# Optimization experiments

Measured on AMD Instinct MI355X. Metric: run time of the kernel, lower is better.

## Reference

```python
import jax, jax.numpy as jnp
import numpy as np

NPG = 128      # nodes per graph = g(4) * e(32), forced by rearrange + cnn1 channels
G, E32 = 4, 32
ALPHA = 1.0    # GCN2Conv(in_channels, 1) -> alpha = 1
BETA = 1.0     # theta=None -> beta = 1


def _gcn_norm(edge_index, edge_weight, n):
    """PyG gcn_norm: add self-loops (w=1), sym-normalize by degree at dst."""
    src, dst = edge_index[0], edge_index[1]
    loop = jnp.arange(n)
    src = jnp.concatenate([src, loop])
    dst = jnp.concatenate([dst, loop])
    w = jnp.concatenate([edge_weight, jnp.ones((n,), edge_weight.dtype)])
    deg = jax.ops.segment_sum(w, dst, num_segments=n)
    dinv = jnp.where(deg > 0, jax.lax.rsqrt(deg), 0.0)
    norm = dinv[src] * w * dinv[dst]
    return src, dst, norm


def _propagate(x, src, dst, norm, n):
    # gather -> weight -> scatter-add (SpMM)
    return jax.ops.segment_sum(x[src] * norm[:, None], dst, num_segments=n)


def setup_inputs() -> dict:
    key = jax.random.key(0)
    ks = jax.random.split(key, 10)
    N, E, C, H, CH = 65536, 524288, 128, 512, 256
    x = jax.random.normal(ks[0], (N, C), jnp.float32)
    edge_index = jax.random.randint(ks[1], (2, E), 0, N, dtype=jnp.int64)
    edge_attr = jax.random.uniform(ks[2], (E,), jnp.float32)
    w1_gcn2 = jax.random.normal(ks[3], (C, C), jnp.float32) / np.float32(np.sqrt(C))
    w_gcn = jax.random.normal(ks[4], (C, H), jnp.float32) / np.float32(np.sqrt(C))
    b_gcn = jnp.zeros((H,), jnp.float32)
    w_cnn1 = jax.random.normal(ks[5], (H, 4 * H), jnp.float32) / np.float32(np.sqrt(4 * H))
    b_cnn1 = jnp.zeros((H,), jnp.float32)
    w_cnn2 = jax.random.normal(ks[6], (CH, H), jnp.float32) / np.float32(np.sqrt(H))
    b_cnn2 = jnp.zeros((CH,), jnp.float32)
    w_lin = jax.random.normal(ks[7], (32 * CH,), jnp.float32) / np.float32(np.sqrt(32 * CH))
    b_lin = jnp.zeros((), jnp.float32)
    return {"x": x, "edge_attr": edge_attr, "w1_gcn2": w1_gcn2, "w_gcn": w_gcn,
            "b_gcn": b_gcn, "w_cnn1": w_cnn1, "b_cnn1": b_cnn1, "w_cnn2": w_cnn2,
            "b_cnn2": b_cnn2, "w_lin": w_lin, "b_lin": b_lin, "edge_index": edge_index}


def reference(x, edge_attr, w1_gcn2, w_gcn, b_gcn, w_cnn1, b_cnn1, w_cnn2, b_cnn2,
              w_lin, b_lin, edge_index):
    n = x.shape[0]
    bs = n // NPG
    src, dst, norm = _gcn_norm(edge_index, edge_attr, n)

    # GCN2Conv(C, layer=1): h = (1-a)*A_hat x + a*x0; out = (1-b)*h + b*(h @ W1)
    h = _propagate(x, src, dst, norm, n)
    h = h * (1.0 - ALPHA) + ALPHA * x
    h = (1.0 - BETA) * h + BETA * (h @ w1_gcn2)

    # GCNConv(C, H): A_hat (h @ W) + b
    h = _propagate(h @ w_gcn, src, dst, norm, n) + b_gcn
    h = jnp.tanh(h)

    f = h.shape[1]  # hidden_channels
    # '(bs g e) f -> bs (g f) e', e=32, g=4
    h = h.reshape(bs, G, E32, f).transpose(0, 1, 3, 2).reshape(bs, G * f, E32)
    # 1x1 convs == per-position linears over channel dim
    h = jax.nn.relu(jnp.einsum('bce,oc->boe', h, w_cnn1) + b_cnn1[None, :, None])
    h = jax.nn.relu(jnp.einsum('bce,oc->boe', h, w_cnn2) + b_cnn2[None, :, None])
    # dropout p=0.5 is identity in eval mode
    h = h.reshape(bs, -1)
    out = h @ w_lin + b_lin
    return jax.nn.sigmoid(out)
```

## Files before the change

kernel.cpp:

```cpp
#include <hip/hip_runtime.h>
#include <hip/hip_bf16.h>

#define N_NODES 65536
#define N_EDGES 524288

typedef __attribute__((ext_vector_type(8))) short bf16x8;
typedef __attribute__((ext_vector_type(4))) float f32x4;

__device__ __forceinline__ float bf2f(unsigned short u) {
    union { unsigned int i; float f; } v;
    v.i = ((unsigned int)u) << 16;
    return v.f;
}
__device__ __forceinline__ unsigned short f2bf(float f) {
    union { float f; unsigned int i; } v;
    v.f = f;
    unsigned int r = v.i + 0x7fff + ((v.i >> 16) & 1);
    return (unsigned short)(r >> 16);
}

__global__ void init_k(int* __restrict__ cnt, float* __restrict__ logits) {
    int i = blockIdx.x * 256 + threadIdx.x;
    cnt[i] = 0;
    if (i < 512) logits[i] = 0.0f;
}
__global__ void cnt_k(const int* __restrict__ dst, int* __restrict__ cnt) {
    int e = blockIdx.x * 256 + threadIdx.x;
    atomicAdd(&cnt[dst[e]], 1);
}

__global__ __launch_bounds__(256) void scan1_k(const int* __restrict__ cnt,
                                               int* __restrict__ rp,
                                               int* __restrict__ bsum) {
    __shared__ int s[256];
    int t = threadIdx.x, g = blockIdx.x * 256 + t;
    int v = cnt[g];
    s[t] = v;
    __syncthreads();
    for (int d = 1; d < 256; d <<= 1) {
        int u = (t >= d) ? s[t - d] : 0;
        __syncthreads();
        s[t] += u;
        __syncthreads();
    }
    rp[g] = s[t] - v;
    if (t == 255) bsum[blockIdx.x] = s[255];
}
__global__ __launch_bounds__(256) void scan2_k(int* __restrict__ bsum,
                                               int* __restrict__ rp) {
    __shared__ int s[256];
    int t = threadIdx.x;
    int v = bsum[t];
    s[t] = v;
    __syncthreads();
    for (int d = 1; d < 256; d <<= 1) {
        int u = (t >= d) ? s[t - d] : 0;
        __syncthreads();
        s[t] += u;
        __syncthreads();
    }
    bsum[t] = s[t] - v;
    if (t == 255) rp[65536] = s[255];
}
__global__ __launch_bounds__(256) void scan3_k(int* __restrict__ rp,
                                               const int* __restrict__ bsum,
                                               int* __restrict__ cursor) {
    int t = threadIdx.x, g = blockIdx.x * 256 + t;
    int r = rp[g] + bsum[blockIdx.x];
    rp[g] = r;
    cursor[g] = r;
}

__global__ void scatter_k(const int* __restrict__ src, const int* __restrict__ dst,
                          const float* __restrict__ w,
                          int* __restrict__ cursor, uint2* __restrict__ ep) {
    int e = blockIdx.x * 256 + threadIdx.x;
    int pos = atomicAdd(&cursor[dst[e]], 1);
    uint2 p;
    p.x = (unsigned int)src[e];
    p.y = __float_as_uint(w[e]);
    ep[pos] = p;
}

__global__ void rowsum_k(const int* __restrict__ rp, const uint2* __restrict__ ep,
                         float* __restrict__ dinv) {
    int n = blockIdx.x * 256 + threadIdx.x;
    int beg = rp[n], end = rp[n + 1];
    float s = 1.0f;
    for (int i = beg; i < end; ++i) s += __uint_as_float(ep[i].y);
    dinv[n] = rsqrtf(s);
}

__global__ void xscale_k(const float* __restrict__ x, const float* __restrict__ dinv,
                         __hip_bfloat16* __restrict__ xbf) {
    int i = (blockIdx.x * 256 + threadIdx.x) * 4;
    float d = dinv[i >> 7];
    float4 v = *(const float4*)(x + i);
    alignas(8) __hip_bfloat16 tmp[4] = {
        __float2bfloat16(d * v.x), __float2bfloat16(d * v.y),
        __float2bfloat16(d * v.z), __float2bfloat16(d * v.w)};
    *(ushort4*)((unsigned short*)xbf + i) = *(const ushort4*)tmp;
}

__global__ void wprep_k(const float* __restrict__ wc1, __hip_bfloat16* __restrict__ wc1bf,
                        const float* __restrict__ wc2, __hip_bfloat16* __restrict__ wc2bf,
                        const float* __restrict__ w1, const float* __restrict__ wg,
                        __hip_bfloat16* __restrict__ WT) {
    int bid = blockIdx.x;
    if (bid < 1152) {
        const float* in;
        __hip_bfloat16* outp;
        int i;
        if (bid < 1024) { in = wc1; outp = wc1bf; i = bid * 1024 + threadIdx.x * 4; }
        else            { in = wc2; outp = wc2bf; i = (bid - 1024) * 1024 + threadIdx.x * 4; }
        float4 v = *(const float4*)(in + i);
        alignas(8) __hip_bfloat16 tmp[4] = {__float2bfloat16(v.x), __float2bfloat16(v.y),
                                            __float2bfloat16(v.z), __float2bfloat16(v.w)};
        *(ushort4*)((unsigned short*)outp + i) = *(const ushort4*)tmp;
    } else {
        int t = (bid - 1152) * 256 + threadIdx.x;
        int f = t >> 7, c = t & 127;
        float s = 0.f;
#pragma unroll 8
        for (int m = 0; m < 128; ++m) s += w1[c * 128 + m] * wg[m * 512 + f];
        WT[t] = __float2bfloat16(s);
    }
}

__global__ __launch_bounds__(256) void gather_k(const int* __restrict__ rp,
                                                const uint2* __restrict__ ep,
                                                const unsigned short* __restrict__ xbf,
                                                const float* __restrict__ dinv,
                                                __hip_bfloat16* __restrict__ ybf) {
    int n = (blockIdx.x * 256 + threadIdx.x) >> 6;
    int lane = threadIdx.x & 63;
    int beg = rp[n], end = rp[n + 1];
    float accx, accy;
    {
        unsigned int u = *(const unsigned int*)(xbf + (size_t)n * 128 + lane * 2);
        accx = bf2f((unsigned short)(u & 0xffff));
        accy = bf2f((unsigned short)(u >> 16));
    }
    int i = beg;
    for (; i + 8 <= end; i += 8) {
        uint2 p[8];
        unsigned int u[8];
#pragma unroll
        for (int k = 0; k < 8; ++k) p[k] = ep[i + k];
#pragma unroll
        for (int k = 0; k < 8; ++k)
            u[k] = *(const unsigned int*)(xbf + (size_t)p[k].x * 128 + lane * 2);
#pragma unroll
        for (int k = 0; k < 8; ++k) {
            float c = __uint_as_float(p[k].y);
            accx += c * bf2f((unsigned short)(u[k] & 0xffff));
            accy += c * bf2f((unsigned short)(u[k] >> 16));
        }
    }
    for (; i + 4 <= end; i += 4) {
        uint2 p[4];
        unsigned int u[4];
#pragma unroll
        for (int k = 0; k < 4; ++k) p[k] = ep[i + k];
#pragma unroll
        for (int k = 0; k < 4; ++k)
            u[k] = *(const unsigned int*)(xbf + (size_t)p[k].x * 128 + lane * 2);
#pragma unroll
        for (int k = 0; k < 4; ++k) {
            float c = __uint_as_float(p[k].y);
            accx += c * bf2f((unsigned short)(u[k] & 0xffff));
            accy += c * bf2f((unsigned short)(u[k] >> 16));
        }
    }
    for (; i < end; ++i) {
        uint2 p = ep[i];
        unsigned int u = *(const unsigned int*)(xbf + (size_t)p.x * 128 + lane * 2);
        float c = __uint_as_float(p.y);
        accx += c * bf2f((unsigned short)(u & 0xffff));
        accy += c * bf2f((unsigned short)(u >> 16));
    }
    float dn = dinv[n];
    accx *= dn;
    accy *= dn;
    alignas(4) __hip_bfloat16 o[2] = {__float2bfloat16(accx), __float2bfloat16(accy)};
    *(unsigned int*)((unsigned short*)ybf + (size_t)n * 128 + lane * 2) =
        *(const unsigned int*)o;
}

__device__ __forceinline__ void gll16(const void* g, void* l) {
    __builtin_amdgcn_global_load_lds(
        (const __attribute__((address_space(1))) void*)g,
        (__attribute__((address_space(3))) void*)l, 16, 0, 0);
}

template <int ACT, int OUT_MODE, int SWIZ_NTX>
__global__ __launch_bounds__(256) void gemm_mfma_k(
    const __hip_bfloat16* __restrict__ A, const __hip_bfloat16* __restrict__ B,
    const float* __restrict__ bias, void* __restrict__ Cout,
    const float* __restrict__ wlin, int M, int N, int K) {
    __shared__ char lds[65536];

    const int tid = threadIdx.x;
    const int lane = tid & 63, wid = tid >> 6;
    int bx, by;
    if (SWIZ_NTX > 0) {
        int orig = blockIdx.x;
        int per = gridDim.x / (8 * SWIZ_NTX);
        int xcd = orig & 7, k = orig >> 3;
        by = xcd * per + k / SWIZ_NTX;
        bx = k % SWIZ_NTX;
    } else {
        bx = blockIdx.x;
        by = blockIdx.y;
    }
    const int bm = by * 128, bn = bx * 128;
    const int wr = wid >> 1, wc = wid & 1;

    const int srow = wid * 16 + (lane >> 2);
    const int skcol = (((lane & 3) ^ ((lane >> 3) & 3))) * 8;
    const __hip_bfloat16* Abase = A + (size_t)(bm + srow) * K + skcol;
    const __hip_bfloat16* Bbase = B + (size_t)(bn + srow) * K + skcol;
    const int ldso = wid * 1024;

    f32x4 acc[4][4] = {};

    const int lrow = lane & 15;
    const int lkb = (((lane >> 4) ^ ((lane >> 1) & 3)) << 4);
    const int nk = K >> 5;

    auto stage = [&](int buf, int kt) {
        char* la = lds + buf * 16384;
        char* lb = la + 8192;
        gll16(Abase + kt * 32,                  la + ldso);
        gll16(Abase + kt * 32 + (size_t)64 * K, la + 4096 + ldso);
        gll16(Bbase + kt * 32,                  lb + ldso);
        gll16(Bbase + kt * 32 + (size_t)64 * K, lb + 4096 + ldso);
    };

    stage(0, 0);
    stage(1, 1);
    stage(2, 2);

    for (int kt = 0; kt < nk; ++kt) {
        int ahead = nk - 1 - kt;
        if (ahead >= 2)      asm volatile("s_waitcnt vmcnt(8)" ::: "memory");
        else if (ahead == 1) asm volatile("s_waitcnt vmcnt(4)" ::: "memory");
        else                 asm volatile("s_waitcnt vmcnt(0)" ::: "memory");
        __builtin_amdgcn_s_barrier();
        asm volatile("" ::: "memory");
        if (kt + 3 < nk) stage((kt + 3) & 3, kt + 3);

        const char* la = lds + (kt & 3) * 16384;
        const char* lb = la + 8192;
        bf16x8 af[4], bfr[4];
#pragma unroll
        for (int i = 0; i < 4; ++i)
            af[i] = *(const bf16x8*)(la + (wr * 64 + i * 16 + lrow) * 64 + lkb);
#pragma unroll
        for (int j = 0; j < 4; ++j)
            bfr[j] = *(const bf16x8*)(lb + (wc * 64 + j * 16 + lrow) * 64 + lkb);
        __builtin_amdgcn_s_setprio(1);
#pragma unroll
        for (int i = 0; i < 4; ++i)
#pragma unroll
            for (int j = 0; j < 4; ++j)
                acc[i][j] = __builtin_amdgcn_mfma_f32_16x16x32_bf16(
                    bfr[j], af[i], acc[i][j], 0, 0, 0);
        __builtin_amdgcn_s_setprio(0);
        asm volatile("" ::: "memory");
    }

    const int l15 = lane & 15, lhi = lane >> 4;

    if (OUT_MODE == 3) {
        float p0 = 0.f, p1 = 0.f;
#pragma unroll
        for (int i = 0; i < 4; ++i) {
            int e = (i & 1) * 16 + l15;
#pragma unroll
            for (int j = 0; j < 4; ++j) {
                int n = bn + wc * 64 + j * 16 + lhi * 4;
                float4 bv = *(const float4*)(bias + n);
#pragma unroll
                for (int r = 0; r < 4; ++r) {
                    float v = fmaxf(acc[i][j][r] + ((const float*)&bv)[r], 0.f);
                    float wl = wlin[(n + r) * 32 + e];
                    if (i < 2) p0 += v * wl; else p1 += v * wl;
                }
            }
        }
#pragma unroll
        for (int off = 32; off > 0; off >>= 1) {
            p0 += __shfl_down(p0, off, 64);
            p1 += __shfl_down(p1, off, 64);
        }
        if (lane == 0) {
            int g = (bm >> 5) + wr * 2;
            atomicAdd(&((float*)Cout)[g], p0);
            atomicAdd(&((float*)Cout)[g + 1], p1);
        }
        return;
    }

#pragma unroll
    for (int i = 0; i < 4; ++i) {
        int m = bm + wr * 64 + i * 16 + l15;
#pragma unroll
        for (int j = 0; j < 4; ++j) {
            int n = bn + wc * 64 + j * 16 + lhi * 4;
            float4 bv = *(const float4*)(bias + n);
            ushort4 o;
#pragma unroll
            for (int r = 0; r < 4; ++r) {
                float v = acc[i][j][r] + ((const float*)&bv)[r];
                if (ACT == 1) v = fmaxf(v, 0.f);
                if (ACT == 2) v = 1.0f - 2.0f / (__expf(2.0f * v) + 1.0f);
                ((unsigned short*)&o)[r] = f2bf(v);
            }
            if (OUT_MODE == 1) {
                *(ushort4*)((unsigned short*)Cout + (size_t)m * N + n) = o;
            } else {
                size_t prow = (size_t)(((m >> 7) << 5) | (m & 31));
                size_t idx = prow * 2048 + (size_t)(((m >> 5) & 3) * 512 + n);
                *(ushort4*)((unsigned short*)Cout + idx) = o;
            }
        }
    }
}

__global__ void sigmoid_k(const float* __restrict__ logits,
                          const float* __restrict__ blin, float* __restrict__ out) {
    int b = blockIdx.x * 256 + threadIdx.x;
    out[b] = 1.0f / (1.0f + expf(-(logits[b] + blin[0])));
}

extern "C" void kernel_launch(void* const* d_in, const int* in_sizes, int n_in,
                              void* d_out, int out_size, void* d_ws, size_t ws_size,
                              hipStream_t stream) {
    const float* x    = (const float*)d_in[0];
    const float* eattr= (const float*)d_in[1];
    const float* w1   = (const float*)d_in[2];
    const float* wg   = (const float*)d_in[3];
    const float* bg   = (const float*)d_in[4];
    const float* wc1  = (const float*)d_in[5];
    const float* bc1  = (const float*)d_in[6];
    const float* wc2  = (const float*)d_in[7];
    const float* bc2  = (const float*)d_in[8];
    const float* wlin = (const float*)d_in[9];
    const float* blin = (const float*)d_in[10];
    const int*   ei   = (const int*)d_in[11];
    const int* esrc = ei;
    const int* edst = ei + N_EDGES;
    float* out = (float*)d_out;

    char* ws = (char*)d_ws;
    float*          dinv   = (float*)(ws + 0);
    int*            cnt    = (int*)(ws + 262144);
    int*            rp     = (int*)(ws + 524288);
    int*            cursor = (int*)(ws + 786688);
    uint2*          ep     = (uint2*)(ws + 1048832);
    __hip_bfloat16* WTbf   = (__hip_bfloat16*)(ws + 5243136);
    __hip_bfloat16* ybf    = (__hip_bfloat16*)(ws + 5374208);
    __hip_bfloat16* V      = (__hip_bfloat16*)(ws + 22151424);
    __hip_bfloat16* act1   = (__hip_bfloat16*)(ws + 89260288);
    __hip_bfloat16* wc1bf  = (__hip_bfloat16*)(ws + 106037504);
    __hip_bfloat16* wc2bf  = (__hip_bfloat16*)(ws + 108134656);
    __hip_bfloat16* xbf    = (__hip_bfloat16*)(ws + 108396800);
    float*          logits = (float*)(ws + 125174016);
    int*            bsum   = (int*)(ws + 125176064);
    if (ws_size < (size_t)125177088) return;

    init_k<<<N_NODES / 256, 256, 0, stream>>>(cnt, logits);

    cnt_k<<<N_EDGES / 256, 256, 0, stream>>>(edst, cnt);

    scan1_k<<<256, 256, 0, stream>>>(cnt, rp, bsum);
    scan2_k<<<1, 256, 0, stream>>>(bsum, rp);
    scan3_k<<<256, 256, 0, stream>>>(rp, bsum, cursor);

    scatter_k<<<N_EDGES / 256, 256, 0, stream>>>(esrc, edst, eattr, cursor, ep);

    rowsum_k<<<N_NODES / 256, 256, 0, stream>>>(rp, ep, dinv);

    wprep_k<<<1408, 256, 0, stream>>>(wc1, wc1bf, wc2, wc2bf, w1, wg, WTbf);
    xscale_k<<<(N_NODES * 128 / 4) / 256, 256, 0, stream>>>(x, dinv, xbf);

    gather_k<<<N_NODES / 4, 256, 0, stream>>>(rp, ep,
                                              (const unsigned short*)xbf, dinv, ybf);

    gemm_mfma_k<2, 2, 0><<<dim3(4, 512), 256, 0, stream>>>(
        ybf, WTbf, bg, V, nullptr, 65536, 512, 128);

    gemm_mfma_k<1, 1, 4><<<512, 256, 0, stream>>>(
        V, wc1bf, bc1, act1, nullptr, 16384, 512, 2048);

    gemm_mfma_k<1, 3, 0><<<dim3(2, 128), 256, 0, stream>>>(
        act1, wc2bf, bc2, logits, wlin, 16384, 256, 512);

    sigmoid_k<<<2, 256, 0, stream>>>(logits, blin, out);
}
```

Measured before the change: 212.7 us.

## Fuse SpMM gather with first GEMM, merge prep and rowsum/xscale kernels

```diff
diff --git a/kernel.cpp b/kernel.cpp
--- a/kernel.cpp
+++ b/kernel.cpp
@@ -24,9 +24,35 @@
     cnt[i] = 0;
     if (i < 512) logits[i] = 0.0f;
 }
-__global__ void cnt_k(const int* __restrict__ dst, int* __restrict__ cnt) {
-    int e = blockIdx.x * 256 + threadIdx.x;
-    atomicAdd(&cnt[dst[e]], 1);
+
+__global__ void prep1_k(const int* __restrict__ dst, int* __restrict__ cnt,
+                        const float* __restrict__ wc1, __hip_bfloat16* __restrict__ wc1bf,
+                        const float* __restrict__ wc2, __hip_bfloat16* __restrict__ wc2bf,
+                        const float* __restrict__ w1, const float* __restrict__ wg,
+                        __hip_bfloat16* __restrict__ WTpk) {
+    int bid = blockIdx.x;
+    if (bid < 2048) {
+        int e = bid * 256 + threadIdx.x;
+        atomicAdd(&cnt[dst[e]], 1);
+    } else if (bid < 3200) {
+        const float* in;
+        __hip_bfloat16* outp;
+        int i;
+        if (bid < 3072) { in = wc1; outp = wc1bf; i = (bid - 2048) * 1024 + threadIdx.x * 4; }
+        else            { in = wc2; outp = wc2bf; i = (bid - 3072) * 1024 + threadIdx.x * 4; }
+        float4 v = *(const float4*)(in + i);
+        alignas(8) __hip_bfloat16 tmp[4] = {__float2bfloat16(v.x), __float2bfloat16(v.y),
+                                            __float2bfloat16(v.z), __float2bfloat16(v.w)};
+        *(ushort4*)((unsigned short*)outp + i) = *(const ushort4*)tmp;
+    } else {
+        int t = (bid - 3200) * 256 + threadIdx.x;
+        int f = t >> 7, c = t & 127;
+        float s = 0.f;
+#pragma unroll 8
+        for (int m = 0; m < 128; ++m) s += w1[c * 128 + m] * wg[m * 512 + f];
+        int pk = ((((f >> 4) * 4 + (c >> 5)) * 64 + ((c >> 3) & 3) * 16 + (f & 15)) * 8) + (c & 7);
+        WTpk[pk] = __float2bfloat16(s);
+    }
 }
 
 __global__ __launch_bounds__(256) void scan1_k(const int* __restrict__ cnt,
@@ -82,109 +108,126 @@
     ep[pos] = p;
 }
 
-__global__ void rowsum_k(const int* __restrict__ rp, const uint2* __restrict__ ep,
-                         float* __restrict__ dinv) {
-    int n = blockIdx.x * 256 + threadIdx.x;
-    int beg = rp[n], end = rp[n + 1];
-    float s = 1.0f;
-    for (int i = beg; i < end; ++i) s += __uint_as_float(ep[i].y);
-    dinv[n] = rsqrtf(s);
-}
-
-__global__ void xscale_k(const float* __restrict__ x, const float* __restrict__ dinv,
-                         __hip_bfloat16* __restrict__ xbf) {
-    int i = (blockIdx.x * 256 + threadIdx.x) * 4;
-    float d = dinv[i >> 7];
-    float4 v = *(const float4*)(x + i);
-    alignas(8) __hip_bfloat16 tmp[4] = {
-        __float2bfloat16(d * v.x), __float2bfloat16(d * v.y),
-        __float2bfloat16(d * v.z), __float2bfloat16(d * v.w)};
-    *(ushort4*)((unsigned short*)xbf + i) = *(const ushort4*)tmp;
-}
-
-__global__ void wprep_k(const float* __restrict__ wc1, __hip_bfloat16* __restrict__ wc1bf,
-                        const float* __restrict__ wc2, __hip_bfloat16* __restrict__ wc2bf,
-                        const float* __restrict__ w1, const float* __restrict__ wg,
-                        __hip_bfloat16* __restrict__ WT) {
-    int bid = blockIdx.x;
-    if (bid < 1152) {
-        const float* in;
-        __hip_bfloat16* outp;
-        int i;
-        if (bid < 1024) { in = wc1; outp = wc1bf; i = bid * 1024 + threadIdx.x * 4; }
-        else            { in = wc2; outp = wc2bf; i = (bid - 1024) * 1024 + threadIdx.x * 4; }
-        float4 v = *(const float4*)(in + i);
-        alignas(8) __hip_bfloat16 tmp[4] = {__float2bfloat16(v.x), __float2bfloat16(v.y),
-                                            __float2bfloat16(v.z), __float2bfloat16(v.w)};
-        *(ushort4*)((unsigned short*)outp + i) = *(const ushort4*)tmp;
-    } else {
-        int t = (bid - 1152) * 256 + threadIdx.x;
-        int f = t >> 7, c = t & 127;
-        float s = 0.f;
-#pragma unroll 8
-        for (int m = 0; m < 128; ++m) s += w1[c * 128 + m] * wg[m * 512 + f];
-        WT[t] = __float2bfloat16(s);
-    }
-}
-
-__global__ __launch_bounds__(256) void gather_k(const int* __restrict__ rp,
-                                                const uint2* __restrict__ ep,
-                                                const unsigned short* __restrict__ xbf,
-                                                const float* __restrict__ dinv,
-                                                __hip_bfloat16* __restrict__ ybf) {
+__global__ __launch_bounds__(256) void rx_k(const int* __restrict__ rp,
+                                            const uint2* __restrict__ ep,
+                                            const float* __restrict__ x,
+                                            float* __restrict__ dinv,
+                                            __hip_bfloat16* __restrict__ xbf) {
     int n = (blockIdx.x * 256 + threadIdx.x) >> 6;
     int lane = threadIdx.x & 63;
     int beg = rp[n], end = rp[n + 1];
-    float accx, accy;
-    {
-        unsigned int u = *(const unsigned int*)(xbf + (size_t)n * 128 + lane * 2);
-        accx = bf2f((unsigned short)(u & 0xffff));
-        accy = bf2f((unsigned short)(u >> 16));
-    }
-    int i = beg;
-    for (; i + 8 <= end; i += 8) {
-        uint2 p[8];
-        unsigned int u[8];
-#pragma unroll
-        for (int k = 0; k < 8; ++k) p[k] = ep[i + k];
-#pragma unroll
-        for (int k = 0; k < 8; ++k)
-            u[k] = *(const unsigned int*)(xbf + (size_t)p[k].x * 128 + lane * 2);
-#pragma unroll
-        for (int k = 0; k < 8; ++k) {
-            float c = __uint_as_float(p[k].y);
-            accx += c * bf2f((unsigned short)(u[k] & 0xffff));
-            accy += c * bf2f((unsigned short)(u[k] >> 16));
-        }
-    }
-    for (; i + 4 <= end; i += 4) {
-        uint2 p[4];
-        unsigned int u[4];
-#pragma unroll
-        for (int k = 0; k < 4; ++k) p[k] = ep[i + k];
-#pragma unroll
-        for (int k = 0; k < 4; ++k)
-            u[k] = *(const unsigned int*)(xbf + (size_t)p[k].x * 128 + lane * 2);
-#pragma unroll
-        for (int k = 0; k < 4; ++k) {
-            float c = __uint_as_float(p[k].y);
-            accx += c * bf2f((unsigned short)(u[k] & 0xffff));
-            accy += c * bf2f((unsigned short)(u[k] >> 16));
-        }
-    }
-    for (; i < end; ++i) {
-        uint2 p = ep[i];
-        unsigned int u = *(const unsigned int*)(xbf + (size_t)p.x * 128 + lane * 2);
-        float c = __uint_as_float(p.y);
-        accx += c * bf2f((unsigned short)(u & 0xffff));
-        accy += c * bf2f((unsigned short)(u >> 16));
-    }
-    float dn = dinv[n];
-    accx *= dn;
-    accy *= dn;
-    alignas(4) __hip_bfloat16 o[2] = {__float2bfloat16(accx), __float2bfloat16(accy)};
-    *(unsigned int*)((unsigned short*)ybf + (size_t)n * 128 + lane * 2) =
+    float s = 0.f;
+    for (int i = beg + lane; i < end; i += 64)
+        s += __uint_as_float(ep[i].y);
+#pragma unroll
+    for (int off = 32; off > 0; off >>= 1) s += __shfl_xor(s, off, 64);
+    float d = rsqrtf(s + 1.0f);
+    if (lane == 0) dinv[n] = d;
+    float2 v = *(const float2*)(x + (size_t)n * 128 + lane * 2);
+    alignas(4) __hip_bfloat16 o[2] = {__float2bfloat16(d * v.x),
+                                      __float2bfloat16(d * v.y)};
+    *(unsigned int*)((unsigned short*)xbf + (size_t)n * 128 + lane * 2) =
         *(const unsigned int*)o;
+}
+
+__global__ __launch_bounds__(256) void gh2_k(
+    const int* __restrict__ rp, const uint2* __restrict__ ep,
+    const unsigned short* __restrict__ xbf, const float* __restrict__ dinv,
+    const __hip_bfloat16* __restrict__ WTpk, const float* __restrict__ bg,
+    __hip_bfloat16* __restrict__ V) {
+    __shared__ char yt[4096];
+    const int tid = threadIdx.x;
+    const int lane = tid & 63, wid = tid >> 6;
+    const int base = blockIdx.x * 16;
+
+    for (int s = 0; s < 4; ++s) {
+        int n = base + wid * 4 + s;
+        int beg = rp[n], end = rp[n + 1];
+        float accx, accy;
+        {
+            unsigned int u = *(const unsigned int*)(xbf + (size_t)n * 128 + lane * 2);
+            accx = bf2f((unsigned short)(u & 0xffff));
+            accy = bf2f((unsigned short)(u >> 16));
+        }
+        int i = beg;
+        for (; i + 8 <= end; i += 8) {
+            uint2 p[8];
+            unsigned int u[8];
+#pragma unroll
+            for (int k = 0; k < 8; ++k) p[k] = ep[i + k];
+#pragma unroll
+            for (int k = 0; k < 8; ++k)
+                u[k] = *(const unsigned int*)(xbf + (size_t)p[k].x * 128 + lane * 2);
+#pragma unroll
+            for (int k = 0; k < 8; ++k) {
+                float c = __uint_as_float(p[k].y);
+                accx += c * bf2f((unsigned short)(u[k] & 0xffff));
+                accy += c * bf2f((unsigned short)(u[k] >> 16));
+            }
+        }
+        for (; i + 4 <= end; i += 4) {
+            uint2 p[4];
+            unsigned int u[4];
+#pragma unroll
+            for (int k = 0; k < 4; ++k) p[k] = ep[i + k];
+#pragma unroll
+            for (int k = 0; k < 4; ++k)
+                u[k] = *(const unsigned int*)(xbf + (size_t)p[k].x * 128 + lane * 2);
+#pragma unroll
+            for (int k = 0; k < 4; ++k) {
+                float c = __uint_as_float(p[k].y);
+                accx += c * bf2f((unsigned short)(u[k] & 0xffff));
+                accy += c * bf2f((unsigned short)(u[k] >> 16));
+            }
+        }
+        for (; i < end; ++i) {
+            uint2 p = ep[i];
+            unsigned int u = *(const unsigned int*)(xbf + (size_t)p.x * 128 + lane * 2);
+            float c = __uint_as_float(p.y);
+            accx += c * bf2f((unsigned short)(u & 0xffff));
+            accy += c * bf2f((unsigned short)(u >> 16));
+        }
+        float dn = dinv[n];
+        int r = wid * 4 + s;
+        int p = (lane >> 2) ^ ((r & 3) << 2);
+        unsigned int o = (unsigned int)f2bf(accx * dn) |
+                         ((unsigned int)f2bf(accy * dn) << 16);
+        *(unsigned int*)(yt + r * 256 + p * 16 + (lane & 3) * 4) = o;
+    }
+    __syncthreads();
+
+    const int l15 = lane & 15, lhi = lane >> 4;
+    const int ar3 = (l15 & 3) << 2;
+    f32x4 acc[8] = {};
+#pragma unroll
+    for (int kt = 0; kt < 4; ++kt) {
+        bf16x8 af = *(const bf16x8*)(yt + l15 * 256 + (((kt * 4 + lhi) ^ ar3) << 4));
+        bf16x8 bfr[8];
+#pragma unroll
+        for (int j = 0; j < 8; ++j)
+            bfr[j] = *(const bf16x8*)(WTpk +
+                ((size_t)((wid * 8 + j) * 4 + kt) * 64 + lane) * 8);
+#pragma unroll
+        for (int j = 0; j < 8; ++j)
+            acc[j] = __builtin_amdgcn_mfma_f32_16x16x32_bf16(
+                bfr[j], af, acc[j], 0, 0, 0);
+    }
+    int m = base + l15;
+    size_t rowbase = ((size_t)(((m >> 7) << 5) | (m & 31))) * 2048 +
+                     (size_t)(((m >> 5) & 3) * 512);
+#pragma unroll
+    for (int j = 0; j < 8; ++j) {
+        int n = wid * 128 + j * 16 + lhi * 4;
+        float4 bv = *(const float4*)(bg + n);
+        ushort4 o;
+#pragma unroll
+        for (int r2 = 0; r2 < 4; ++r2) {
+            float v = acc[j][r2] + ((const float*)&bv)[r2];
+            v = 1.0f - 2.0f / (__expf(2.0f * v) + 1.0f);
+            ((unsigned short*)&o)[r2] = f2bf(v);
+        }
+        *(ushort4*)((unsigned short*)V + rowbase + n) = o;
+    }
 }
 
 __device__ __forceinline__ void gll16(const void* g, void* l) {
@@ -314,16 +357,9 @@
             for (int r = 0; r < 4; ++r) {
                 float v = acc[i][j][r] + ((const float*)&bv)[r];
                 if (ACT == 1) v = fmaxf(v, 0.f);
-                if (ACT == 2) v = 1.0f - 2.0f / (__expf(2.0f * v) + 1.0f);
                 ((unsigned short*)&o)[r] = f2bf(v);
             }
-            if (OUT_MODE == 1) {
-                *(ushort4*)((unsigned short*)Cout + (size_t)m * N + n) = o;
-            } else {
-                size_t prow = (size_t)(((m >> 7) << 5) | (m & 31));
-                size_t idx = prow * 2048 + (size_t)(((m >> 5) & 3) * 512 + n);
-                *(ushort4*)((unsigned short*)Cout + idx) = o;
-            }
+            *(ushort4*)((unsigned short*)Cout + (size_t)m * N + n) = o;
         }
     }
 }
@@ -359,8 +395,7 @@
     int*            rp     = (int*)(ws + 524288);
     int*            cursor = (int*)(ws + 786688);
     uint2*          ep     = (uint2*)(ws + 1048832);
-    __hip_bfloat16* WTbf   = (__hip_bfloat16*)(ws + 5243136);
-    __hip_bfloat16* ybf    = (__hip_bfloat16*)(ws + 5374208);
+    __hip_bfloat16* WTpk   = (__hip_bfloat16*)(ws + 5243136);
     __hip_bfloat16* V      = (__hip_bfloat16*)(ws + 22151424);
     __hip_bfloat16* act1   = (__hip_bfloat16*)(ws + 89260288);
     __hip_bfloat16* wc1bf  = (__hip_bfloat16*)(ws + 106037504);
@@ -372,7 +407,8 @@
 
     init_k<<<N_NODES / 256, 256, 0, stream>>>(cnt, logits);
 
-    cnt_k<<<N_EDGES / 256, 256, 0, stream>>>(edst, cnt);
+    prep1_k<<<3456, 256, 0, stream>>>(edst, cnt, wc1, wc1bf, wc2, wc2bf,
+                                      w1, wg, WTpk);
 
     scan1_k<<<256, 256, 0, stream>>>(cnt, rp, bsum);
     scan2_k<<<1, 256, 0, stream>>>(bsum, rp);
@@ -380,16 +416,10 @@
 
     scatter_k<<<N_EDGES / 256, 256, 0, stream>>>(esrc, edst, eattr, cursor, ep);
 
-    rowsum_k<<<N_NODES / 256, 256, 0, stream>>>(rp, ep, dinv);
-
-    wprep_k<<<1408, 256, 0, stream>>>(wc1, wc1bf, wc2, wc2bf, w1, wg, WTbf);
-    xscale_k<<<(N_NODES * 128 / 4) / 256, 256, 0, stream>>>(x, dinv, xbf);
-
-    gather_k<<<N_NODES / 4, 256, 0, stream>>>(rp, ep,
-                                              (const unsigned short*)xbf, dinv, ybf);
-
-    gemm_mfma_k<2, 2, 0><<<dim3(4, 512), 256, 0, stream>>>(
-        ybf, WTbf, bg, V, nullptr, 65536, 512, 128);
+    rx_k<<<N_NODES / 4, 256, 0, stream>>>(rp, ep, x, dinv, xbf);
+
+    gh2_k<<<N_NODES / 16, 256, 0, stream>>>(rp, ep, (const unsigned short*)xbf,
+                                            dinv, WTpk, bg, V);
 
     gemm_mfma_k<1, 1, 4><<<512, 256, 0, stream>>>(
         V, wc1bf, bc1, act1, nullptr, 16384, 512, 2048);
```

Result: slower. 218.7 us (+2.8%).

## Add dedicated cnn1 GEMM kernel with pre-packed B fragments loaded directly to registers

Applied to the files above, without the earlier changes.

```diff
diff --git a/kernel.cpp b/kernel.cpp
--- a/kernel.cpp
+++ b/kernel.cpp
@@ -102,23 +102,31 @@
     *(ushort4*)((unsigned short*)xbf + i) = *(const ushort4*)tmp;
 }
 
-__global__ void wprep_k(const float* __restrict__ wc1, __hip_bfloat16* __restrict__ wc1bf,
+__global__ void wprep_k(const float* __restrict__ wc1, __hip_bfloat16* __restrict__ wc1pk,
                         const float* __restrict__ wc2, __hip_bfloat16* __restrict__ wc2bf,
                         const float* __restrict__ w1, const float* __restrict__ wg,
                         __hip_bfloat16* __restrict__ WT) {
     int bid = blockIdx.x;
-    if (bid < 1152) {
-        const float* in;
-        __hip_bfloat16* outp;
-        int i;
-        if (bid < 1024) { in = wc1; outp = wc1bf; i = bid * 1024 + threadIdx.x * 4; }
-        else            { in = wc2; outp = wc2bf; i = (bid - 1024) * 1024 + threadIdx.x * 4; }
-        float4 v = *(const float4*)(in + i);
+    if (bid < 512) {
+        int t = bid * 256 + threadIdx.x;
+        int l = t & 63, grp = t >> 6;
+        int kt = grp & 63, nb = grp >> 6;
+        int n = nb * 16 + (l & 15);
+        int k0 = kt * 32 + (l >> 4) * 8;
+        const float* src = wc1 + (size_t)n * 2048 + k0;
+        alignas(16) __hip_bfloat16 tmp[8];
+#pragma unroll
+        for (int e = 0; e < 8; ++e) tmp[e] = __float2bfloat16(src[e]);
+        *(ushort4*)((unsigned short*)wc1pk + (size_t)t * 8)     = *(const ushort4*)tmp;
+        *(ushort4*)((unsigned short*)wc1pk + (size_t)t * 8 + 4) = *(const ushort4*)(tmp + 4);
+    } else if (bid < 640) {
+        int i = (bid - 512) * 1024 + threadIdx.x * 4;
+        float4 v = *(const float4*)(wc2 + i);
         alignas(8) __hip_bfloat16 tmp[4] = {__float2bfloat16(v.x), __float2bfloat16(v.y),
                                             __float2bfloat16(v.z), __float2bfloat16(v.w)};
-        *(ushort4*)((unsigned short*)outp + i) = *(const ushort4*)tmp;
+        *(ushort4*)((unsigned short*)wc2bf + i) = *(const ushort4*)tmp;
     } else {
-        int t = (bid - 1152) * 256 + threadIdx.x;
+        int t = (bid - 640) * 256 + threadIdx.x;
         int f = t >> 7, c = t & 127;
         float s = 0.f;
 #pragma unroll 8
@@ -324,6 +332,113 @@
                 size_t idx = prow * 2048 + (size_t)(((m >> 5) & 3) * 512 + n);
                 *(ushort4*)((unsigned short*)Cout + idx) = o;
             }
+        }
+    }
+}
+
+__global__ __launch_bounds__(512) void cnn1w_k(
+    const __hip_bfloat16* __restrict__ A,
+    const __hip_bfloat16* __restrict__ Bpk,
+    const float* __restrict__ bias,
+    __hip_bfloat16* __restrict__ C) {
+    __shared__ char lds[16384];
+    const int tid = threadIdx.x;
+    const int lane = tid & 63, wid = tid >> 6;
+    const int bm = blockIdx.x * 64;
+    const int K = 2048, nk = 64;
+    const bool stager = (wid < 4);
+
+    const int srow = (wid & 3) * 16 + (lane >> 2);
+    const int skcol = (((lane & 3) ^ ((lane >> 3) & 3))) * 8;
+    const __hip_bfloat16* Abase = A + (size_t)(bm + srow) * K + skcol;
+    const int ldso = (wid & 3) * 1024;
+
+    const __hip_bfloat16* Bp[4];
+#pragma unroll
+    for (int j = 0; j < 4; ++j)
+        Bp[j] = Bpk + ((size_t)(wid * 4 + j) * nk) * 512 + lane * 8;
+
+    f32x4 acc[4][4] = {};
+    const int lrow = lane & 15;
+    const int lkb = (((lane >> 4) ^ ((lane >> 1) & 3)) << 4);
+
+    auto stageA = [&](int buf, int kt) {
+        if (stager) gll16(Abase + kt * 32, lds + buf * 4096 + ldso);
+    };
+
+    bf16x8 b0[4], b1[4];
+    stageA(0, 0);
+    stageA(1, 1);
+    asm volatile("" ::: "memory");
+#pragma unroll
+    for (int j = 0; j < 4; ++j) b0[j] = *(const bf16x8*)(Bp[j]);
+
+#define GEMM_W(KT, BREG)                                                        \
+    {                                                                           \
+        const char* la = lds + ((KT) & 3) * 4096;                               \
+        bf16x8 af[4];                                                           \
+        _Pragma("unroll")                                                       \
+        for (int i = 0; i < 4; ++i)                                             \
+            af[i] = *(const bf16x8*)(la + (i * 16 + lrow) * 64 + lkb);          \
+        __builtin_amdgcn_s_setprio(1);                                          \
+        _Pragma("unroll")                                                       \
+        for (int i = 0; i < 4; ++i)                                             \
+            _Pragma("unroll")                                                   \
+            for (int j = 0; j < 4; ++j)                                         \
+                acc[i][j] = __builtin_amdgcn_mfma_f32_16x16x32_bf16(            \
+                    BREG[j], af[i], acc[i][j], 0, 0, 0);                        \
+        __builtin_amdgcn_s_setprio(0);                                          \
+        asm volatile("" ::: "memory");                                          \
+    }
+
+    for (int kt = 0; kt < nk; kt += 2) {
+        if (kt + 2 < nk) stageA((kt + 2) & 3, kt + 2);
+#pragma unroll
+        for (int j = 0; j < 4; ++j)
+            b1[j] = *(const bf16x8*)(Bp[j] + (size_t)(kt + 1) * 512);
+        if (stager) {
+            if (kt + 2 < nk) asm volatile("s_waitcnt vmcnt(5)" ::: "memory");
+            else             asm volatile("s_waitcnt vmcnt(4)" ::: "memory");
+        } else {
+            asm volatile("s_waitcnt vmcnt(4)" ::: "memory");
+        }
+        __builtin_amdgcn_s_barrier();
+        asm volatile("" ::: "memory");
+        GEMM_W(kt, b0);
+
+        if (kt + 3 < nk) stageA((kt + 3) & 3, kt + 3);
+        if (kt + 2 < nk) {
+#pragma unroll
+            for (int j = 0; j < 4; ++j)
+                b0[j] = *(const bf16x8*)(Bp[j] + (size_t)(kt + 2) * 512);
+        }
+        if (kt + 2 < nk) {
+            if (stager) asm volatile("s_waitcnt vmcnt(5)" ::: "memory");
+            else        asm volatile("s_waitcnt vmcnt(4)" ::: "memory");
+        } else {
+            asm volatile("s_waitcnt vmcnt(0)" ::: "memory");
+        }
+        __builtin_amdgcn_s_barrier();
+        asm volatile("" ::: "memory");
+        GEMM_W(kt + 1, b1);
+    }
+#undef GEMM_W
+
+    const int l15 = lane & 15, lhi = lane >> 4;
+#pragma unroll
+    for (int i = 0; i < 4; ++i) {
+        int m = bm + i * 16 + l15;
+#pragma unroll
+        for (int j = 0; j < 4; ++j) {
+            int n = wid * 64 + j * 16 + lhi * 4;
+            float4 bv = *(const float4*)(bias + n);
+            ushort4 o;
+#pragma unroll
+            for (int r = 0; r < 4; ++r) {
+                float v = fmaxf(acc[i][j][r] + ((const float*)&bv)[r], 0.f);
+                ((unsigned short*)&o)[r] = f2bf(v);
+            }
+            *(ushort4*)((unsigned short*)C + (size_t)m * 512 + n) = o;
         }
     }
 }
@@ -363,7 +478,7 @@
     __hip_bfloat16* ybf    = (__hip_bfloat16*)(ws + 5374208);
     __hip_bfloat16* V      = (__hip_bfloat16*)(ws + 22151424);
     __hip_bfloat16* act1   = (__hip_bfloat16*)(ws + 89260288);
-    __hip_bfloat16* wc1bf  = (__hip_bfloat16*)(ws + 106037504);
+    __hip_bfloat16* wc1pk  = (__hip_bfloat16*)(ws + 106037504);
     __hip_bfloat16* wc2bf  = (__hip_bfloat16*)(ws + 108134656);
     __hip_bfloat16* xbf    = (__hip_bfloat16*)(ws + 108396800);
     float*          logits = (float*)(ws + 125174016);
@@ -382,7 +497,7 @@
 
     rowsum_k<<<N_NODES / 256, 256, 0, stream>>>(rp, ep, dinv);
 
-    wprep_k<<<1408, 256, 0, stream>>>(wc1, wc1bf, wc2, wc2bf, w1, wg, WTbf);
+    wprep_k<<<896, 256, 0, stream>>>(wc1, wc1pk, wc2, wc2bf, w1, wg, WTbf);
     xscale_k<<<(N_NODES * 128 / 4) / 256, 256, 0, stream>>>(x, dinv, xbf);
 
     gather_k<<<N_NODES / 4, 256, 0, stream>>>(rp, ep,
@@ -391,8 +506,7 @@
     gemm_mfma_k<2, 2, 0><<<dim3(4, 512), 256, 0, stream>>>(
         ybf, WTbf, bg, V, nullptr, 65536, 512, 128);
 
-    gemm_mfma_k<1, 1, 4><<<512, 256, 0, stream>>>(
-        V, wc1bf, bc1, act1, nullptr, 16384, 512, 2048);
+    cnn1w_k<<<256, 512, 0, stream>>>(V, wc1pk, bc1, act1);
 
     gemm_mfma_k<1, 3, 0><<<dim3(2, 128), 256, 0, stream>>>(
         act1, wc2bf, bc2, logits, wlin, 16384, 256, 512);
```

Measured after the change: 210.3 us. About the same (-1.2%).

## Fuse GCN weight GEMM with tanh and cnn1 GEMM, keeping hidden tile in LDS

Applied to the files above, without the earlier changes.

```diff
diff --git a/kernel.cpp b/kernel.cpp
--- a/kernel.cpp
+++ b/kernel.cpp
@@ -102,28 +102,37 @@
     *(ushort4*)((unsigned short*)xbf + i) = *(const ushort4*)tmp;
 }
 
-__global__ void wprep_k(const float* __restrict__ wc1, __hip_bfloat16* __restrict__ wc1bf,
+__global__ void wprep_k(const float* __restrict__ wc1, __hip_bfloat16* __restrict__ wc1pk,
                         const float* __restrict__ wc2, __hip_bfloat16* __restrict__ wc2bf,
                         const float* __restrict__ w1, const float* __restrict__ wg,
-                        __hip_bfloat16* __restrict__ WT) {
+                        __hip_bfloat16* __restrict__ WTpk) {
     int bid = blockIdx.x;
-    if (bid < 1152) {
-        const float* in;
-        __hip_bfloat16* outp;
-        int i;
-        if (bid < 1024) { in = wc1; outp = wc1bf; i = bid * 1024 + threadIdx.x * 4; }
-        else            { in = wc2; outp = wc2bf; i = (bid - 1024) * 1024 + threadIdx.x * 4; }
-        float4 v = *(const float4*)(in + i);
+    if (bid < 512) {
+        int t = bid * 256 + threadIdx.x;
+        int l = t & 63, grp = t >> 6;
+        int kt = grp & 63, nb = grp >> 6;
+        int n = nb * 16 + (l & 15);
+        int k0 = kt * 32 + (l >> 4) * 8;
+        const float* src = wc1 + (size_t)n * 2048 + k0;
+        alignas(16) __hip_bfloat16 tmp[8];
+#pragma unroll
+        for (int e = 0; e < 8; ++e) tmp[e] = __float2bfloat16(src[e]);
+        *(ushort4*)((unsigned short*)wc1pk + (size_t)t * 8)     = *(const ushort4*)tmp;
+        *(ushort4*)((unsigned short*)wc1pk + (size_t)t * 8 + 4) = *(const ushort4*)(tmp + 4);
+    } else if (bid < 640) {
+        int i = (bid - 512) * 1024 + threadIdx.x * 4;
+        float4 v = *(const float4*)(wc2 + i);
         alignas(8) __hip_bfloat16 tmp[4] = {__float2bfloat16(v.x), __float2bfloat16(v.y),
                                             __float2bfloat16(v.z), __float2bfloat16(v.w)};
-        *(ushort4*)((unsigned short*)outp + i) = *(const ushort4*)tmp;
+        *(ushort4*)((unsigned short*)wc2bf + i) = *(const ushort4*)tmp;
     } else {
-        int t = (bid - 1152) * 256 + threadIdx.x;
+        int t = (bid - 640) * 256 + threadIdx.x;
         int f = t >> 7, c = t & 127;
         float s = 0.f;
 #pragma unroll 8
         for (int m = 0; m < 128; ++m) s += w1[c * 128 + m] * wg[m * 512 + f];
-        WT[t] = __float2bfloat16(s);
+        int pk = ((((f >> 4) * 4 + (c >> 5)) * 64 + ((c >> 3) & 3) * 16 + (f & 15)) * 8) + (c & 7);
+        WTpk[pk] = __float2bfloat16(s);
     }
 }
 
@@ -193,6 +202,149 @@
         (__attribute__((address_space(3))) void*)l, 16, 0, 0);
 }
 
+__global__ __launch_bounds__(512) void fh2c1_k(
+    const __hip_bfloat16* __restrict__ ybf,
+    const __hip_bfloat16* __restrict__ WTpk,
+    const float* __restrict__ bg,
+    const __hip_bfloat16* __restrict__ wc1pk,
+    const float* __restrict__ bc1,
+    __hip_bfloat16* __restrict__ act1) {
+    __shared__ char yt[16384];
+    __shared__ char ht[65536];
+    const int tid = threadIdx.x;
+    const int lane = tid & 63, wid = tid >> 6;
+    const int bx = blockIdx.x;
+    const int l15 = lane & 15, lhi = lane >> 4;
+
+    const __hip_bfloat16* Bp[4];
+#pragma unroll
+    for (int j = 0; j < 4; ++j)
+        Bp[j] = wc1pk + ((size_t)(wid * 4 + j) * 64) * 512 + lane * 8;
+
+    f32x4 acc[4][4] = {};
+
+    for (int g = 0; g < 4; ++g) {
+        __syncthreads();
+#pragma unroll
+        for (int q = 0; q < 2; ++q) {
+            int a = wid * 8 + q * 4 + (lane >> 4);
+            int node = bx * 256 + ((a >> 5) << 7) + g * 32 + (a & 31);
+            int scol = ((lane & 15) ^ (a & 7)) << 4;
+            gll16((const char*)ybf + (size_t)node * 256 + scol,
+                  yt + wid * 2048 + q * 1024 + lane * 16);
+        }
+        __syncthreads();
+
+        {
+            f32x4 hacc[4][4] = {};
+#pragma unroll
+            for (int kt = 0; kt < 4; ++kt) {
+                bf16x8 af[4], bfr[4];
+#pragma unroll
+                for (int i = 0; i < 4; ++i) {
+                    int r = i * 16 + l15;
+                    int s = (kt * 4 + lhi) ^ (r & 7);
+                    af[i] = *(const bf16x8*)(yt + r * 256 + s * 16);
+                }
+#pragma unroll
+                for (int j = 0; j < 4; ++j)
+                    bfr[j] = *(const bf16x8*)(WTpk +
+                        ((size_t)((wid * 4 + j) * 4 + kt) * 64 + lane) * 8);
+#pragma unroll
+                for (int i = 0; i < 4; ++i)
+#pragma unroll
+                    for (int j = 0; j < 4; ++j)
+                        hacc[i][j] = __builtin_amdgcn_mfma_f32_16x16x32_bf16(
+                            bfr[j], af[i], hacc[i][j], 0, 0, 0);
+            }
+#pragma unroll
+            for (int j = 0; j < 4; ++j) {
+                float4 bgv = *(const float4*)(bg + wid * 64 + j * 16 + lhi * 4);
+                int bytecol = wid * 128 + j * 32 + lhi * 8;
+                int s = bytecol >> 4;
+                int off8 = bytecol & 15;
+#pragma unroll
+                for (int i = 0; i < 4; ++i) {
+                    int row = i * 16 + l15;
+                    alignas(8) unsigned short o[4];
+#pragma unroll
+                    for (int r = 0; r < 4; ++r) {
+                        float v = hacc[i][j][r] + ((const float*)&bgv)[r];
+                        v = 1.0f - 2.0f / (__expf(2.0f * v) + 1.0f);
+                        o[r] = f2bf(v);
+                    }
+                    *(uint2*)(ht + row * 1024 + ((s ^ (row & 7)) << 4) + off8) =
+                        *(const uint2*)o;
+                }
+            }
+        }
+        __syncthreads();
+
+        bf16x8 b0[4], b1[4];
+#pragma unroll
+        for (int j = 0; j < 4; ++j)
+            b0[j] = *(const bf16x8*)(Bp[j] + (size_t)(g * 16) * 512);
+#pragma unroll
+        for (int kk = 0; kk < 16; kk += 2) {
+#pragma unroll
+            for (int j = 0; j < 4; ++j)
+                b1[j] = *(const bf16x8*)(Bp[j] + (size_t)(g * 16 + kk + 1) * 512);
+            {
+                bf16x8 af[4];
+#pragma unroll
+                for (int i = 0; i < 4; ++i) {
+                    int r = i * 16 + l15;
+                    int s = (kk * 4 + lhi) ^ (r & 7);
+                    af[i] = *(const bf16x8*)(ht + r * 1024 + s * 16);
+                }
+#pragma unroll
+                for (int i = 0; i < 4; ++i)
+#pragma unroll
+                    for (int j = 0; j < 4; ++j)
+                        acc[i][j] = __builtin_amdgcn_mfma_f32_16x16x32_bf16(
+                            b0[j], af[i], acc[i][j], 0, 0, 0);
+            }
+            if (kk + 2 < 16) {
+#pragma unroll
+                for (int j = 0; j < 4; ++j)
+                    b0[j] = *(const bf16x8*)(Bp[j] + (size_t)(g * 16 + kk + 2) * 512);
+            }
+            {
+                bf16x8 af[4];
+#pragma unroll
+                for (int i = 0; i < 4; ++i) {
+                    int r = i * 16 + l15;
+                    int s = ((kk + 1) * 4 + lhi) ^ (r & 7);
+                    af[i] = *(const bf16x8*)(ht + r * 1024 + s * 16);
+                }
+#pragma unroll
+                for (int i = 0; i < 4; ++i)
+#pragma unroll
+                    for (int j = 0; j < 4; ++j)
+                        acc[i][j] = __builtin_amdgcn_mfma_f32_16x16x32_bf16(
+                            b1[j], af[i], acc[i][j], 0, 0, 0);
+            }
+        }
+    }
+
+#pragma unroll
+    for (int i = 0; i < 4; ++i) {
+        int m = bx * 64 + i * 16 + l15;
+#pragma unroll
+        for (int j = 0; j < 4; ++j) {
+            int n = wid * 64 + j * 16 + lhi * 4;
+            float4 bv = *(const float4*)(bc1 + n);
+            ushort4 o;
+#pragma unroll
+            for (int r = 0; r < 4; ++r) {
+                float v = fmaxf(acc[i][j][r] + ((const float*)&bv)[r], 0.f);
+                ((unsigned short*)&o)[r] = f2bf(v);
+            }
+            *(ushort4*)((unsigned short*)act1 + (size_t)m * 512 + n) = o;
+        }
+    }
+}
+
 template <int ACT, int OUT_MODE, int SWIZ_NTX>
 __global__ __launch_bounds__(256) void gemm_mfma_k(
     const __hip_bfloat16* __restrict__ A, const __hip_bfloat16* __restrict__ B,
@@ -314,16 +466,9 @@
             for (int r = 0; r < 4; ++r) {
                 float v = acc[i][j][r] + ((const float*)&bv)[r];
                 if (ACT == 1) v = fmaxf(v, 0.f);
-                if (ACT == 2) v = 1.0f - 2.0f / (__expf(2.0f * v) + 1.0f);
                 ((unsigned short*)&o)[r] = f2bf(v);
             }
-            if (OUT_MODE == 1) {
-                *(ushort4*)((unsigned short*)Cout + (size_t)m * N + n) = o;
-            } else {
-                size_t prow = (size_t)(((m >> 7) << 5) | (m & 31));
-                size_t idx = prow * 2048 + (size_t)(((m >> 5) & 3) * 512 + n);
-                *(ushort4*)((unsigned short*)Cout + idx) = o;
-            }
+            *(ushort4*)((unsigned short*)Cout + (size_t)m * N + n) = o;
         }
     }
 }
@@ -359,11 +504,10 @@
     int*            rp     = (int*)(ws + 524288);
     int*            cursor = (int*)(ws + 786688);
     uint2*          ep     = (uint2*)(ws + 1048832);
-    __hip_bfloat16* WTbf   = (__hip_bfloat16*)(ws + 5243136);
+    __hip_bfloat16* WTpk   = (__hip_bfloat16*)(ws + 5243136);
     __hip_bfloat16* ybf    = (__hip_bfloat16*)(ws + 5374208);
-    __hip_bfloat16* V      = (__hip_bfloat16*)(ws + 22151424);
     __hip_bfloat16* act1   = (__hip_bfloat16*)(ws + 89260288);
-    __hip_bfloat16* wc1bf  = (__hip_bfloat16*)(ws + 106037504);
+    __hip_bfloat16* wc1pk  = (__hip_bfloat16*)(ws + 106037504);
     __hip_bfloat16* wc2bf  = (__hip_bfloat16*)(ws + 108134656);
     __hip_bfloat16* xbf    = (__hip_bfloat16*)(ws + 108396800);
     float*          logits = (float*)(ws + 125174016);
@@ -382,17 +526,13 @@
 
     rowsum_k<<<N_NODES / 256, 256, 0, stream>>>(rp, ep, dinv);
 
-    wprep_k<<<1408, 256, 0, stream>>>(wc1, wc1bf, wc2, wc2bf, w1, wg, WTbf);
+    wprep_k<<<896, 256, 0, stream>>>(wc1, wc1pk, wc2, wc2bf, w1, wg, WTpk);
     xscale_k<<<(N_NODES * 128 / 4) / 256, 256, 0, stream>>>(x, dinv, xbf);
 
     gather_k<<<N_NODES / 4, 256, 0, stream>>>(rp, ep,
                                               (const unsigned short*)xbf, dinv, ybf);
 
-    gemm_mfma_k<2, 2, 0><<<dim3(4, 512), 256, 0, stream>>>(
-        ybf, WTbf, bg, V, nullptr, 65536, 512, 128);
-
-    gemm_mfma_k<1, 1, 4><<<512, 256, 0, stream>>>(
-        V, wc1bf, bc1, act1, nullptr, 16384, 512, 2048);
+    fh2c1_k<<<256, 512, 0, stream>>>(ybf, WTpk, bg, wc1pk, bc1, act1);
 
     gemm_mfma_k<1, 3, 0><<<dim3(2, 128), 256, 0, stream>>>(
         act1, wc2bf, bc2, logits, wlin, 16384, 256, 512);
```

Measured after the change: 200.6 us. 1.06x faster.
